# Kernel optimization log

Measured on AMD Instinct MI355X. Metric: run time of the kernel, lower is better.

Reference implementation:

```python
import jax, jax.numpy as jnp
import numpy as np

B, N, F_IN = 4, 2048, 256
K, D = 4, 64
NEG_SLOPE = 0.2


def setup_inputs() -> dict:
    key = jax.random.key(0)
    k1, k2, k3, k4, k5 = jax.random.split(key, 5)
    x = jax.random.normal(k1, (B, N, F_IN), dtype=jnp.float32)
    adj = jax.random.randint(k2, (B, N, N), 0, 2, dtype=jnp.int32)
    # xavier_uniform-style params
    def xavier(k, shape):
        fan_in, fan_out = shape[-2], shape[-1]
        lim = np.sqrt(6.0 / (fan_in + fan_out))
        return jax.random.uniform(k, shape, jnp.float32, -lim, lim)
    W = xavier(k3, (K, F_IN, D))
    a_src = xavier(k4, (K, D, 1))
    a_dst = xavier(k5, (K, D, 1))
    return {"x": x, "adj": adj, "W": W, "a_src": a_src, "a_dst": a_dst}


def reference(x, adj, W, a_src, a_dst):
    # Wh: (B, K, N, D)
    Wh = jnp.einsum('bnf,kfd->bknd', x, W)
    e_src = jnp.einsum('bknd,kdo->bkno', Wh, a_src)  # (B,K,N,1)
    e_dst = jnp.einsum('bknd,kdo->bkno', Wh, a_dst)  # (B,K,N,1)
    e = e_src + jnp.swapaxes(e_dst, -2, -1)          # (B,K,N,N)
    e = jnp.where(e > 0, e, NEG_SLOPE * e)           # LeakyReLU(0.2)
    # adjacency mask with forced self-loops (adj + I > 0)
    eye = jnp.eye(e.shape[-1], dtype=bool)
    mask = (adj[:, None, :, :] > 0) | eye            # (B,1|K,N,N)
    e = jnp.where(mask, e, -jnp.inf)
    # numerically-stable softmax matching F_module_softmax
    x_max = jnp.max(e, axis=-1, keepdims=True)
    x_max = jnp.where(jnp.isinf(x_max), 0.0, x_max)
    exp_e = jnp.exp(e - x_max)
    exp_e = jnp.where(jnp.isinf(e), 0.0, exp_e)
    alpha = exp_e / (jnp.sum(exp_e, axis=-1, keepdims=True) + 1e-10)
    # dropout is identity in eval mode
    out = jnp.matmul(alpha, Wh)                      # (B,K,N,D)
    # concat heads: (B,N,K*D)
    Bn, Kn, Nn, Dn = out.shape
    return jnp.transpose(out, (0, 2, 1, 3)).reshape(Bn, Nn, Kn * Dn)
```

## Files before the change

kernel.cpp:

```cpp
#include <hip/hip_runtime.h>

#define NB 4
#define NN 2048
#define NF 256
#define NK 4
#define ND 64
#define NEG 0.2f
#define LOG2E 1.4426950408889634f

typedef _Float16 f16;
typedef _Float16 f16x4 __attribute__((ext_vector_type(4)));
typedef _Float16 f16x8 __attribute__((ext_vector_type(8)));
typedef float f32x4 __attribute__((ext_vector_type(4)));
typedef float f32x16 __attribute__((ext_vector_type(16)));

__device__ __forceinline__ int gsz(int d) { return (d ^ (d >> 3)) & 7; }

__global__ __launch_bounds__(256) void k01(
    const float* __restrict__ x,
    const int*   __restrict__ adj,
    const float* __restrict__ Wm,
    const float* __restrict__ a_src,
    const float* __restrict__ a_dst,
    unsigned int* __restrict__ abit,
    f16* __restrict__ wht,
    float* __restrict__ sbuf,
    float* __restrict__ ebuf,
    float* __restrict__ fbuf)
{
    __shared__ f16 wt[64 * 256];

    const int bx  = blockIdx.x;
    const int tid = threadIdx.x;

    if (bx >= 256) {
        const int row = (bx - 256) * 4 + (tid >> 6);
        const int l   = tid & 63;
        const int i   = row & (NN - 1);
        const int* __restrict__ ar = adj + (size_t)row * NN;

        int v[32];
#pragma unroll
        for (int c = 0; c < 32; ++c) v[c] = ar[c * 64 + l];

        unsigned int kx = 0, ky = 0;
#pragma unroll
        for (int c = 0; c < 32; ++c) {
            unsigned long long m = __ballot(v[c] > 0);
            if (l == c) { kx = (unsigned int)m; ky = (unsigned int)(m >> 32); }
        }
        if (l == (i >> 6)) {
            unsigned int sb = 1u << (i & 31);
            if (((i >> 5) & 1) == 0) kx |= sb; else ky |= sb;
        }
        if (l < 32) {
            uint2 kk; kk.x = kx; kk.y = ky;
            *(uint2*)&abit[(size_t)row * 64 + l * 2] = kk;
        }
        return;
    }

    const int gx  = bx & 15;
    const int k   = (bx >> 4) & 3;
    const int b   = bx >> 6;
    const int wv  = tid >> 6;
    const int l   = tid & 63;
    const int q   = l >> 4;
    const int r16 = l & 15;

    for (int fc = 0; fc < 64; ++fc) {
        int f = fc * 4 + wv;
        int d = l;
        wt[d * 256 + (f ^ ((d & 7) << 3))] = (f16)Wm[(k * NF + f) * ND + d];
    }
    __syncthreads();

    const int ncol0 = gx * 128 + wv * 32;
    f32x4 acc[2][4];
#pragma unroll
    for (int nt = 0; nt < 2; ++nt)
#pragma unroll
        for (int dt = 0; dt < 4; ++dt)
            acc[nt][dt] = (f32x4){0.f, 0.f, 0.f, 0.f};

    for (int fs = 0; fs < 16; ++fs) {
        const int f0 = fs * 16 + q * 4;
        f16x4 af[4];
#pragma unroll
        for (int dt = 0; dt < 4; ++dt) {
            int d = dt * 16 + r16;
            af[dt] = *(const f16x4*)&wt[d * 256 + (f0 ^ ((d & 7) << 3))];
        }
#pragma unroll
        for (int nt = 0; nt < 2; ++nt) {
            int n = ncol0 + nt * 16 + r16;
            float4 xv = *(const float4*)&x[((size_t)(b * NN + n)) * NF + f0];
            f16x4 bf = {(f16)xv.x, (f16)xv.y, (f16)xv.z, (f16)xv.w};
#pragma unroll
            for (int dt = 0; dt < 4; ++dt)
                acc[nt][dt] = __builtin_amdgcn_mfma_f32_16x16x16f16(
                    af[dt], bf, acc[nt][dt], 0, 0, 0);
        }
    }

    float asv[4][4], adv[4][4];
#pragma unroll
    for (int dt = 0; dt < 4; ++dt)
#pragma unroll
        for (int rr = 0; rr < 4; ++rr) {
            int d = dt * 16 + q * 4 + rr;
            asv[dt][rr] = a_src[k * ND + d];
            adv[dt][rr] = a_dst[k * ND + d];
        }

    const size_t obase = (size_t)(b * NK + k) * 131072;

#pragma unroll
    for (int nt = 0; nt < 2; ++nt) {
        int n  = ncol0 + nt * 16 + r16;
        int s_ = n >> 6, g = (n >> 3) & 7, e = n & 7;
        float sp = 0.f, tp = 0.f;
#pragma unroll
        for (int dt = 0; dt < 4; ++dt)
#pragma unroll
            for (int rr = 0; rr < 4; ++rr) {
                float v = acc[nt][dt][rr];
                int d = dt * 16 + q * 4 + rr;
                wht[obase + s_ * 4096 + d * 64 + ((g ^ gsz(d)) << 3) + e] = (f16)v;
                sp += v * asv[dt][rr];
                tp += v * adv[dt][rr];
            }
        sp += __shfl_xor(sp, 16);
        sp += __shfl_xor(sp, 32);
        tp += __shfl_xor(tp, 16);
        tp += __shfl_xor(tp, 32);
        if (q == 0) {
            int idx = (b * NK + k) * NN + n;
            sbuf[idx] = sp;
            ebuf[idx] = __builtin_exp2f(tp * LOG2E);
            fbuf[idx] = __builtin_exp2f(0.2f * LOG2E * tp);
        }
    }
}

__global__ __launch_bounds__(1024, 4) void k2_attn(
    const unsigned int* __restrict__ abit,
    const f16* __restrict__ wht,
    const float* __restrict__ sbuf,
    const float* __restrict__ ebuf,
    const float* __restrict__ fbuf,
    float* __restrict__ out)
{
    const int i0  = blockIdx.x * 128;
    const int k   = blockIdx.y;
    const int b   = blockIdx.z;
    const int tid = threadIdx.x;
    const int w   = tid >> 6;
    const int c   = w >> 2;
    const int rw  = w & 3;
    const int l   = tid & 63;
    const int r32 = l & 31;
    const int hi  = l >> 5;
    const int iglob = i0 + rw * 32 + r32;

    __shared__ __attribute__((aligned(16))) char pool[116736];
    float* el   = (float*)(pool + 98304);
    float* fl   = (float*)(pool + 106496);
    float* dden = (float*)(pool + 114688);

    const unsigned int* __restrict__ abrow =
        abit + (size_t)(b * NN + iglob) * 64 + c * 16;
    uint2 abx[8];
#pragma unroll
    for (int it = 0; it < 8; ++it) abx[it] = *(const uint2*)(abrow + it * 2);

    {
        const float* eb = ebuf + (b * NK + k) * NN;
        const float* fb = fbuf + (b * NK + k) * NN;
        int t5 = tid & 511;
        if (tid < 512) *(float4*)&el[t5 * 4] = *(const float4*)&eb[t5 * 4];
        else           *(float4*)&fl[t5 * 4] = *(const float4*)&fb[t5 * 4];
    }

    const float s  = sbuf[(b * NK + k) * NN + iglob];
    const float Af = __builtin_exp2f(0.8f * LOG2E * fminf(s, 0.f));
    const float Bf = __builtin_exp2f(-0.8f * LOG2E * fmaxf(s, 0.f));
    const char* gtiles = (const char*)wht + (size_t)(b * NK + k) * 262144;

    float denom = 0.f;
    f32x16 acc[2];
#pragma unroll
    for (int dh = 0; dh < 2; ++dh)
#pragma unroll
        for (int z = 0; z < 16; ++z) acc[dh][z] = 0.f;

#define STAGE8(bb, it)                                                         \
    do {                                                                       \
        const char* gsrc = gtiles + (size_t)(c * 8 + (it)) * 8192 +            \
                           (tid & 255) * 16;                                   \
        char* ldst = pool + c * 24576 + (bb) * 8192 + (tid & 255) * 16;        \
        __builtin_amdgcn_global_load_lds(                                      \
            (const __attribute__((address_space(1))) void*)gsrc,               \
            (__attribute__((address_space(3))) void*)ldst, 16, 0, 0);          \
        __builtin_amdgcn_global_load_lds(                                      \
            (const __attribute__((address_space(1))) void*)(gsrc + 4096),      \
            (__attribute__((address_space(3))) void*)(ldst + 4096), 16, 0, 0); \
    } while (0)

    __builtin_amdgcn_sched_barrier(0);
    STAGE8(0, 0);
    STAGE8(1, 1);

#pragma unroll
    for (int it = 0; it < 8; ++it) {
        if (it < 7) asm volatile("s_waitcnt vmcnt(2) lgkmcnt(0)" ::: "memory");
        else        asm volatile("s_waitcnt vmcnt(0) lgkmcnt(0)" ::: "memory");
        __builtin_amdgcn_sched_barrier(0);
        __builtin_amdgcn_s_barrier();
        __builtin_amdgcn_sched_barrier(0);
        if (it < 6) STAGE8((it + 2) % 3, it + 2);

        const char* lb = pool + c * 24576 + (it % 3) * 8192;
        const uint2 ab = abx[it];
#pragma unroll
        for (int jj = 0; jj < 4; ++jj) {
            const int jts = (jj + c) & 3;
            const unsigned int word  = (jts & 2) ? ab.y : ab.x;
            const unsigned int mbyte = (word >> (((jts & 1) << 4) + (hi << 3))) & 0xffu;
            const int jb = c * 512 + it * 64 + jts * 16 + hi * 8;
            float4 e0 = *(const float4*)&el[jb];
            float4 e1 = *(const float4*)&el[jb + 4];
            float4 f0 = *(const float4*)&fl[jb];
            float4 f1 = *(const float4*)&fl[jb + 4];
            float ev[8] = {e0.x, e0.y, e0.z, e0.w, e1.x, e1.y, e1.z, e1.w};
            float fv[8] = {f0.x, f0.y, f0.z, f0.w, f1.x, f1.y, f1.z, f1.w};
            float wv[8];
#pragma unroll
            for (int e = 0; e < 8; ++e) {
                float m = fmaxf(Af * ev[e], Bf * fv[e]);
                wv[e] = (mbyte & (1u << e)) ? m : 0.f;
            }
            denom += ((wv[0] + wv[1]) + (wv[2] + wv[3])) +
                     ((wv[4] + wv[5]) + (wv[6] + wv[7]));
            f16x8 pa = {(f16)wv[0], (f16)wv[1], (f16)wv[2], (f16)wv[3],
                        (f16)wv[4], (f16)wv[5], (f16)wv[6], (f16)wv[7]};
#pragma unroll
            for (int dh = 0; dh < 2; ++dh) {
                const int d = dh * 32 + r32;
                f16x8 v8 = *(const f16x8*)(lb + d * 128 +
                               ((((jts << 1) | hi) ^ gsz(d)) << 4));
                acc[dh] = __builtin_amdgcn_mfma_f32_32x32x16_f16(
                    pa, v8, acc[dh], 0, 0, 0);
            }
        }
    }
#undef STAGE8

    denom += __shfl_xor(denom, 32);

    __syncthreads();
    float* stash = (float*)pool;
    if (c != 0) {
        float* sb = stash + ((c - 1) * 4 + rw) * 2048 + l * 16;
#pragma unroll
        for (int dh = 0; dh < 2; ++dh)
#pragma unroll
            for (int sub = 0; sub < 4; ++sub) {
                f32x4 v = {acc[dh][sub * 4], acc[dh][sub * 4 + 1],
                           acc[dh][sub * 4 + 2], acc[dh][sub * 4 + 3]};
                *(f32x4*)&sb[dh * 1024 + ((sub ^ (l & 3)) << 2)] = v;
            }
    }
    if (l < 32) dden[c * 128 + rw * 32 + l] = denom;
    __syncthreads();

    if (c == 0) {
#pragma unroll
        for (int cc = 0; cc < 3; ++cc) {
            const float* sr = stash + (cc * 4 + rw) * 2048 + l * 16;
#pragma unroll
            for (int dh = 0; dh < 2; ++dh)
#pragma unroll
                for (int sub = 0; sub < 4; ++sub) {
                    f32x4 v = *(const f32x4*)&sr[dh * 1024 + ((sub ^ (l & 3)) << 2)];
#pragma unroll
                    for (int m = 0; m < 4; ++m) acc[dh][sub * 4 + m] += v[m];
                }
        }
        float* op = out + ((size_t)(b * NN) + i0 + rw * 32) * (NK * ND) + k * ND;
#pragma unroll
        for (int g4 = 0; g4 < 4; ++g4) {
            f32x4 ds = {0.f, 0.f, 0.f, 0.f};
#pragma unroll
            for (int c4 = 0; c4 < 4; ++c4) {
                f32x4 dv = *(const f32x4*)&dden[c4 * 128 + rw * 32 + g4 * 8 + hi * 4];
#pragma unroll
                for (int m = 0; m < 4; ++m) ds[m] += dv[m];
            }
#pragma unroll
            for (int m = 0; m < 4; ++m) {
                const int rr   = g4 * 4 + m;
                const int irow = g4 * 8 + hi * 4 + m;
                const float inv = 1.f / (ds[m] + 1e-10f);
                op[(size_t)irow * (NK * ND) + r32]      = acc[0][rr] * inv;
                op[(size_t)irow * (NK * ND) + 32 + r32] = acc[1][rr] * inv;
            }
        }
    }
}

extern "C" void kernel_launch(void* const* d_in, const int* in_sizes, int n_in,
                              void* d_out, int out_size, void* d_ws, size_t ws_size,
                              hipStream_t stream) {
    const float* x     = (const float*)d_in[0];
    const int*   adj   = (const int*)d_in[1];
    const float* Wm    = (const float*)d_in[2];
    const float* a_src = (const float*)d_in[3];
    const float* a_dst = (const float*)d_in[4];
    float* out = (float*)d_out;

    char* ws = (char*)d_ws;
    f16*   wht  = (f16*)ws;
    float* sbuf = (float*)(ws + (4u << 20));
    float* ebuf = (float*)(ws + (4u << 20) + (128u << 10));
    float* fbuf = (float*)(ws + (4u << 20) + (256u << 10));
    unsigned int* abit = (unsigned int*)(ws + (4u << 20) + (384u << 10));

    k01<<<dim3(256 + NB * NN / 4), 256, 0, stream>>>(
        x, adj, Wm, a_src, a_dst, abit, wht, sbuf, ebuf, fbuf);
    k2_attn<<<dim3(NN / 128, NK, NB), 1024, 0, stream>>>(
        abit, wht, sbuf, ebuf, fbuf, out);
}
```

Baseline: 46.38 us.

## Compute attention weights in packed fp16 and shrink attention blocks to 64 rows

Stores the exp(e_dst) factors as fp16 and computes the masked attention weights with packed half2 multiply/max. The adjacency bits are expanded into half2 masks by integer arithmetic, and the denominator is accumulated with fdot2. The attention kernel moves from 1024 to 512 threads with 64 rows per block, doubling the block count and cutting LDS so more blocks can be resident. It also drops from triple to double buffering of the value tiles with a full wait each iteration, which may reduce load/compute overlap. The fp16 weights add rounding and overflow risk for large exponentials.

```diff
diff --git a/kernel.cpp b/kernel.cpp
--- a/kernel.cpp
+++ b/kernel.cpp
@@ -9,10 +9,13 @@
 #define LOG2E 1.4426950408889634f
 
 typedef _Float16 f16;
+typedef _Float16 f16x2 __attribute__((ext_vector_type(2)));
 typedef _Float16 f16x4 __attribute__((ext_vector_type(4)));
 typedef _Float16 f16x8 __attribute__((ext_vector_type(8)));
 typedef float f32x4 __attribute__((ext_vector_type(4)));
 typedef float f32x16 __attribute__((ext_vector_type(16)));
+typedef unsigned int u32;
+typedef unsigned short u16;
 
 __device__ __forceinline__ int gsz(int d) { return (d ^ (d >> 3)) & 7; }
 
@@ -25,8 +28,8 @@
     unsigned int* __restrict__ abit,
     f16* __restrict__ wht,
     float* __restrict__ sbuf,
-    float* __restrict__ ebuf,
-    float* __restrict__ fbuf)
+    f16* __restrict__ ebuf,
+    f16* __restrict__ fbuf)
 {
     __shared__ f16 wt[64 * 256];
 
@@ -137,36 +140,36 @@
         if (q == 0) {
             int idx = (b * NK + k) * NN + n;
             sbuf[idx] = sp;
-            ebuf[idx] = __builtin_exp2f(tp * LOG2E);
-            fbuf[idx] = __builtin_exp2f(0.2f * LOG2E * tp);
+            ebuf[idx] = (f16)__builtin_exp2f(tp * LOG2E);
+            fbuf[idx] = (f16)__builtin_exp2f(0.2f * LOG2E * tp);
         }
     }
 }
 
-__global__ __launch_bounds__(1024, 4) void k2_attn(
+__global__ __launch_bounds__(512, 4) void k2_attn(
     const unsigned int* __restrict__ abit,
     const f16* __restrict__ wht,
     const float* __restrict__ sbuf,
-    const float* __restrict__ ebuf,
-    const float* __restrict__ fbuf,
+    const f16* __restrict__ ebuf,
+    const f16* __restrict__ fbuf,
     float* __restrict__ out)
 {
-    const int i0  = blockIdx.x * 128;
+    const int i0  = blockIdx.x * 64;
     const int k   = blockIdx.y;
     const int b   = blockIdx.z;
     const int tid = threadIdx.x;
     const int w   = tid >> 6;
-    const int c   = w >> 2;
-    const int rw  = w & 3;
+    const int c   = w >> 1;
+    const int rw  = w & 1;
     const int l   = tid & 63;
     const int r32 = l & 31;
     const int hi  = l >> 5;
     const int iglob = i0 + rw * 32 + r32;
 
-    __shared__ __attribute__((aligned(16))) char pool[116736];
-    float* el   = (float*)(pool + 98304);
-    float* fl   = (float*)(pool + 106496);
-    float* dden = (float*)(pool + 114688);
+    __shared__ __attribute__((aligned(16))) char pool[74752];
+    u16*   el   = (u16*)(pool + 65536);
+    u16*   fl   = (u16*)(pool + 69632);
+    float* dden = (float*)(pool + 73728);
 
     const unsigned int* __restrict__ abrow =
         abit + (size_t)(b * NN + iglob) * 64 + c * 16;
@@ -175,16 +178,19 @@
     for (int it = 0; it < 8; ++it) abx[it] = *(const uint2*)(abrow + it * 2);
 
     {
-        const float* eb = ebuf + (b * NK + k) * NN;
-        const float* fb = fbuf + (b * NK + k) * NN;
-        int t5 = tid & 511;
-        if (tid < 512) *(float4*)&el[t5 * 4] = *(const float4*)&eb[t5 * 4];
-        else           *(float4*)&fl[t5 * 4] = *(const float4*)&fb[t5 * 4];
-    }
-
-    const float s  = sbuf[(b * NK + k) * NN + iglob];
-    const float Af = __builtin_exp2f(0.8f * LOG2E * fminf(s, 0.f));
-    const float Bf = __builtin_exp2f(-0.8f * LOG2E * fmaxf(s, 0.f));
+        const u16* eb = (const u16*)(ebuf + (b * NK + k) * NN);
+        const u16* fb = (const u16*)(fbuf + (b * NK + k) * NN);
+        *(ushort4*)&el[tid * 4] = *(const ushort4*)&eb[tid * 4];
+        *(ushort4*)&fl[tid * 4] = *(const ushort4*)&fb[tid * 4];
+    }
+
+    const float s   = sbuf[(b * NK + k) * NN + iglob];
+    const float Aff = __builtin_exp2f(0.8f * LOG2E * fminf(s, 0.f));
+    const float Bff = __builtin_exp2f(-0.8f * LOG2E * fmaxf(s, 0.f));
+    const f16 Afh = (f16)Aff, Bfh = (f16)Bff;
+    const f16x2 Af2 = {Afh, Afh};
+    const f16x2 Bf2 = {Bfh, Bfh};
+    const f16x2 one2 = {(f16)1.0f, (f16)1.0f};
     const char* gtiles = (const char*)wht + (size_t)(b * NK + k) * 262144;
 
     float denom = 0.f;
@@ -197,53 +203,51 @@
 #define STAGE8(bb, it)                                                         \
     do {                                                                       \
         const char* gsrc = gtiles + (size_t)(c * 8 + (it)) * 8192 +            \
-                           (tid & 255) * 16;                                   \
-        char* ldst = pool + c * 24576 + (bb) * 8192 + (tid & 255) * 16;        \
-        __builtin_amdgcn_global_load_lds(                                      \
-            (const __attribute__((address_space(1))) void*)gsrc,               \
-            (__attribute__((address_space(3))) void*)ldst, 16, 0, 0);          \
-        __builtin_amdgcn_global_load_lds(                                      \
-            (const __attribute__((address_space(1))) void*)(gsrc + 4096),      \
-            (__attribute__((address_space(3))) void*)(ldst + 4096), 16, 0, 0); \
+                           rw * 1024 + l * 16;                                 \
+        char* ldst = pool + c * 16384 + (bb) * 8192 + rw * 1024 + l * 16;      \
+        _Pragma("unroll") for (int kk = 0; kk < 4; ++kk)                       \
+            __builtin_amdgcn_global_load_lds(                                  \
+                (const __attribute__((address_space(1))) void*)(gsrc +         \
+                    kk * 2048),                                                \
+                (__attribute__((address_space(3))) void*)(ldst + kk * 2048),   \
+                16, 0, 0);                                                     \
     } while (0)
 
-    __builtin_amdgcn_sched_barrier(0);
     STAGE8(0, 0);
-    STAGE8(1, 1);
 
 #pragma unroll
     for (int it = 0; it < 8; ++it) {
-        if (it < 7) asm volatile("s_waitcnt vmcnt(2) lgkmcnt(0)" ::: "memory");
-        else        asm volatile("s_waitcnt vmcnt(0) lgkmcnt(0)" ::: "memory");
+        asm volatile("s_waitcnt vmcnt(0) lgkmcnt(0)" ::: "memory");
         __builtin_amdgcn_sched_barrier(0);
         __builtin_amdgcn_s_barrier();
         __builtin_amdgcn_sched_barrier(0);
-        if (it < 6) STAGE8((it + 2) % 3, it + 2);
-
-        const char* lb = pool + c * 24576 + (it % 3) * 8192;
+        if (it < 7) STAGE8((it + 1) & 1, it + 1);
+
+        const char* lb = pool + c * 16384 + (it & 1) * 8192;
         const uint2 ab = abx[it];
 #pragma unroll
-        for (int jj = 0; jj < 4; ++jj) {
-            const int jts = (jj + c) & 3;
-            const unsigned int word  = (jts & 2) ? ab.y : ab.x;
-            const unsigned int mbyte = (word >> (((jts & 1) << 4) + (hi << 3))) & 0xffu;
+        for (int jts = 0; jts < 4; ++jts) {
+            const u32 word = (jts & 2) ? ab.y : ab.x;
+            const u32 bbyte = (word >> (((jts & 1) << 4) + (hi << 3))) & 0xffu;
+            const u32 u = bbyte * 0x8001u;
             const int jb = c * 512 + it * 64 + jts * 16 + hi * 8;
-            float4 e0 = *(const float4*)&el[jb];
-            float4 e1 = *(const float4*)&el[jb + 4];
-            float4 f0 = *(const float4*)&fl[jb];
-            float4 f1 = *(const float4*)&fl[jb + 4];
-            float ev[8] = {e0.x, e0.y, e0.z, e0.w, e1.x, e1.y, e1.z, e1.w};
-            float fv[8] = {f0.x, f0.y, f0.z, f0.w, f1.x, f1.y, f1.z, f1.w};
-            float wv[8];
-#pragma unroll
-            for (int e = 0; e < 8; ++e) {
-                float m = fmaxf(Af * ev[e], Bf * fv[e]);
-                wv[e] = (mbyte & (1u << e)) ? m : 0.f;
-            }
-            denom += ((wv[0] + wv[1]) + (wv[2] + wv[3])) +
-                     ((wv[4] + wv[5]) + (wv[6] + wv[7]));
-            f16x8 pa = {(f16)wv[0], (f16)wv[1], (f16)wv[2], (f16)wv[3],
-                        (f16)wv[4], (f16)wv[5], (f16)wv[6], (f16)wv[7]};
+            uint4 E4 = *(const uint4*)&el[jb];
+            uint4 F4 = *(const uint4*)&fl[jb];
+            u32 pa_u[4];
+#pragma unroll
+            for (int p = 0; p < 4; ++p) {
+                f16x2 e2 = __builtin_bit_cast(f16x2, ((const u32*)&E4)[p]);
+                f16x2 f2 = __builtin_bit_cast(f16x2, ((const u32*)&F4)[p]);
+                f16x2 w2 = __builtin_elementwise_max(Af2 * e2, Bf2 * f2);
+                u32 x  = (u >> (2 * p)) & 0x00010001u;
+                u32 mm = x * 0xffffu;
+                u32 wu = __builtin_bit_cast(u32, w2) & mm;
+                pa_u[p] = wu;
+                denom = __builtin_amdgcn_fdot2(
+                    __builtin_bit_cast(f16x2, wu), one2, denom, false);
+            }
+            uint4 pav = {pa_u[0], pa_u[1], pa_u[2], pa_u[3]};
+            f16x8 pa = __builtin_bit_cast(f16x8, pav);
 #pragma unroll
             for (int dh = 0; dh < 2; ++dh) {
                 const int d = dh * 32 + r32;
@@ -261,28 +265,28 @@
     __syncthreads();
     float* stash = (float*)pool;
     if (c != 0) {
-        float* sb = stash + ((c - 1) * 4 + rw) * 2048 + l * 16;
+        float* sb = stash + ((c - 1) * 2 + rw) * 2048 + l * 32;
 #pragma unroll
         for (int dh = 0; dh < 2; ++dh)
 #pragma unroll
             for (int sub = 0; sub < 4; ++sub) {
                 f32x4 v = {acc[dh][sub * 4], acc[dh][sub * 4 + 1],
                            acc[dh][sub * 4 + 2], acc[dh][sub * 4 + 3]};
-                *(f32x4*)&sb[dh * 1024 + ((sub ^ (l & 3)) << 2)] = v;
-            }
-    }
-    if (l < 32) dden[c * 128 + rw * 32 + l] = denom;
+                *(f32x4*)&sb[dh * 16 + ((sub ^ (l & 3)) << 2)] = v;
+            }
+    }
+    if (hi == 0) dden[c * 64 + rw * 32 + r32] = denom;
     __syncthreads();
 
     if (c == 0) {
 #pragma unroll
         for (int cc = 0; cc < 3; ++cc) {
-            const float* sr = stash + (cc * 4 + rw) * 2048 + l * 16;
+            const float* sr = stash + (cc * 2 + rw) * 2048 + l * 32;
 #pragma unroll
             for (int dh = 0; dh < 2; ++dh)
 #pragma unroll
                 for (int sub = 0; sub < 4; ++sub) {
-                    f32x4 v = *(const f32x4*)&sr[dh * 1024 + ((sub ^ (l & 3)) << 2)];
+                    f32x4 v = *(const f32x4*)&sr[dh * 16 + ((sub ^ (l & 3)) << 2)];
 #pragma unroll
                     for (int m = 0; m < 4; ++m) acc[dh][sub * 4 + m] += v[m];
                 }
@@ -293,7 +297,7 @@
             f32x4 ds = {0.f, 0.f, 0.f, 0.f};
 #pragma unroll
             for (int c4 = 0; c4 < 4; ++c4) {
-                f32x4 dv = *(const f32x4*)&dden[c4 * 128 + rw * 32 + g4 * 8 + hi * 4];
+                f32x4 dv = *(const f32x4*)&dden[c4 * 64 + rw * 32 + g4 * 8 + hi * 4];
 #pragma unroll
                 for (int m = 0; m < 4; ++m) ds[m] += dv[m];
             }
@@ -322,12 +326,12 @@
     char* ws = (char*)d_ws;
     f16*   wht  = (f16*)ws;
     float* sbuf = (float*)(ws + (4u << 20));
-    float* ebuf = (float*)(ws + (4u << 20) + (128u << 10));
-    float* fbuf = (float*)(ws + (4u << 20) + (256u << 10));
-    unsigned int* abit = (unsigned int*)(ws + (4u << 20) + (384u << 10));
+    f16*   ebuf = (f16*)(ws + (4u << 20) + (128u << 10));
+    f16*   fbuf = (f16*)(ws + (4u << 20) + (192u << 10));
+    unsigned int* abit = (unsigned int*)(ws + (4u << 20) + (256u << 10));
 
     k01<<<dim3(256 + NB * NN / 4), 256, 0, stream>>>(
         x, adj, Wm, a_src, a_dst, abit, wht, sbuf, ebuf, fbuf);
-    k2_attn<<<dim3(NN / 128, NK, NB), 1024, 0, stream>>>(
+    k2_attn<<<dim3(NN / 64, NK, NB), 512, 0, stream>>>(
         abit, wht, sbuf, ebuf, fbuf, out);
 }
```

Result: faster. 42.71 us (-7.9%).
